# Performance work log

Hardware: AMD Instinct MI355X
Metric: run time of the kernel (lower is better)

The kernel has to match this reference:

```python
import jax, jax.numpy as jnp
import numpy as np

# Larq ste_sign: forward sign(x) with sign(0)=+1; backward is identity clipped to |x|<=1 (STE).
@jax.custom_vjp
def ste_sign(x):
    return jnp.where(x >= 0, jnp.ones((), x.dtype), -jnp.ones((), x.dtype))

def _ste_fwd(x):
    return ste_sign(x), x

def _ste_bwd(x, g):
    return (g * (jnp.abs(x) <= 1).astype(g.dtype),)

ste_sign.defvjp(_ste_fwd, _ste_bwd)


def setup_inputs() -> dict:
    key = jax.random.key(0)
    k1, k2 = jax.random.split(key)
    x = jax.random.normal(k1, (16, 112, 112, 256), dtype=jnp.float32)      # NHWC
    kernel = jax.random.normal(k2, (3, 3, 256, 1), dtype=jnp.float32) * 0.1  # (kh, kw, C, mult)
    return {"x": x, "kernel": kernel}


def reference(x, kernel):
    # Quantize input and depthwise kernel, then standard depthwise conv (stride 1, SAME, no bias).
    xq = ste_sign(x)
    kq = ste_sign(kernel)
    kh, kw, C, mult = kernel.shape
    rhs = kq.reshape(kh, kw, 1, C * mult)  # HWIO layout for grouped conv
    out = jax.lax.conv_general_dilated(
        xq, rhs,
        window_strides=(1, 1),
        padding="SAME",
        feature_group_count=C,
        dimension_numbers=("NHWC", "HWIO", "NHWC"),
    )
    return out
```

## Files before the change

### kernel.cpp

```cpp
#include <hip/hip_runtime.h>


constexpr int N = 16, H = 112, W = 112, C = 256;
constexpr int TW = 16;

typedef float f32x4 __attribute__((ext_vector_type(4)));

template<bool TOP, bool BOT>
__device__ __forceinline__ void run_strip(
        const float* __restrict__ x, const float* __restrict__ k,
        float* __restrict__ out, int n, int h, int w0, int c0) {

    constexpr unsigned VMASK = (TOP ? 0x1u : 0u) | 0x8u | (BOT ? 0x40u : 0u);
    constexpr int NROWS = (TOP ? 1 : 0) + 1 + (BOT ? 1 : 0);

    unsigned kb[4] = {0u, 0u, 0u, 0u};
#pragma unroll
    for (int t = 0; t < 9; ++t) {
        const uint4 kv = *reinterpret_cast<const uint4*>(k + t * C + c0);
        kb[0] |= (kv.x >> 31) << t;
        kb[1] |= (kv.y >> 31) << t;
        kb[2] |= (kv.z >> 31) << t;
        kb[3] |= (kv.w >> 31) << t;
    }
    unsigned kbj[3][4];
#pragma unroll
    for (int j = 0; j < 3; ++j)
#pragma unroll
        for (int ch = 0; ch < 4; ++ch)
            kbj[j][ch] = (kb[ch] >> j) & 0x49u & VMASK;

    const size_t rowstride = (size_t)W * C;
    const float* rc = x + (size_t)(n * H + h) * rowstride + c0;
    const float* rm = rc - rowstride;
    const float* rp = rc + rowstride;
    float* orow = out + (size_t)(n * H + h) * rowstride + c0;

    auto colD = [&](int cc, int dj[3][4]) {
        uint4 xm = make_uint4(0,0,0,0), xp = make_uint4(0,0,0,0);
        if constexpr (TOP) xm = *reinterpret_cast<const uint4*>(rm + (size_t)cc * C);
        const uint4 xc = *reinterpret_cast<const uint4*>(rc + (size_t)cc * C);
        if constexpr (BOT) xp = *reinterpret_cast<const uint4*>(rp + (size_t)cc * C);

        unsigned xcode[4];
        {
            const unsigned* m = &xm.x; const unsigned* c = &xc.x; const unsigned* p = &xp.x;
#pragma unroll
            for (int ch = 0; ch < 4; ++ch) {
                unsigned r = (c[ch] >> 31) << 3;
                if constexpr (TOP) r |= (m[ch] >> 31);
                if constexpr (BOT) r |= (p[ch] >> 31) << 6;
                xcode[ch] = r;
            }
        }
#pragma unroll
        for (int ch = 0; ch < 4; ++ch)
#pragma unroll
            for (int j = 0; j < 3; ++j)
                dj[j][ch] = NROWS - 2 * __popc(xcode[ch] ^ kbj[j][ch]);
    };

    int d0_m2[4], d0_m1[4], d1_m1[4];

    if (w0 > 0) {
        int dj[3][4]; colD(w0 - 1, dj);
#pragma unroll
        for (int ch = 0; ch < 4; ++ch) d0_m2[ch] = dj[0][ch];
    } else {
#pragma unroll
        for (int ch = 0; ch < 4; ++ch) d0_m2[ch] = 0;
    }
    {
        int dj[3][4]; colD(w0, dj);
#pragma unroll
        for (int ch = 0; ch < 4; ++ch) { d0_m1[ch] = dj[0][ch]; d1_m1[ch] = dj[1][ch]; }
    }

#pragma unroll 3
    for (int i = 1; i < TW; ++i) {
        const int cc = w0 + i;
        int dj[3][4]; colD(cc, dj);
        f32x4 ov;
#pragma unroll
        for (int ch = 0; ch < 4; ++ch) {
            ov[ch] = (float)(d0_m2[ch] + d1_m1[ch] + dj[2][ch]);
            d0_m2[ch] = d0_m1[ch]; d0_m1[ch] = dj[0][ch]; d1_m1[ch] = dj[1][ch];
        }
        __builtin_nontemporal_store(ov,
            reinterpret_cast<f32x4*>(orow + (size_t)(cc - 1) * C));
    }

    {
        const int cc = w0 + TW;
        int d2v[4] = {0, 0, 0, 0};
        if (cc < W) {
            int dj[3][4]; colD(cc, dj);
#pragma unroll
            for (int ch = 0; ch < 4; ++ch) d2v[ch] = dj[2][ch];
        }
        f32x4 ov;
#pragma unroll
        for (int ch = 0; ch < 4; ++ch) ov[ch] = (float)(d0_m2[ch] + d1_m1[ch] + d2v[ch]);
        __builtin_nontemporal_store(ov,
            reinterpret_cast<f32x4*>(orow + (size_t)(cc - 1) * C));
    }
}

__global__ __launch_bounds__(256) void bsign_dw3x3_pop(
        const float* __restrict__ x, const float* __restrict__ k,
        float* __restrict__ out) {
    const int c0 = (threadIdx.x & 63) << 2;
    const int wq = threadIdx.x >> 6;
    const int h  = blockIdx.y * 4 + wq;
    const int w0 = blockIdx.x * TW;
    const int n  = blockIdx.z;

    if (h == 0)            run_strip<false, true >(x, k, out, n, h, w0, c0);
    else if (h == H - 1)   run_strip<true,  false>(x, k, out, n, h, w0, c0);
    else                   run_strip<true,  true >(x, k, out, n, h, w0, c0);
}

extern "C" void kernel_launch(void* const* d_in, const int* in_sizes, int n_in,
                              void* d_out, int out_size, void* d_ws, size_t ws_size,
                              hipStream_t stream) {
    const float* x = (const float*)d_in[0];
    const float* k = (const float*)d_in[1];
    float* out = (float*)d_out;

    dim3 grid(W / TW, H / 4, N);
    bsign_dw3x3_pop<<<grid, 256, 0, stream>>>(x, k, out);
}
```

Measured before the change: 351.3 us.

## Register-block four output rows per thread to cut vertical input re-reads

New measurement: 362.2 us. 1.03x slower.

```diff
diff --git a/kernel.cpp b/kernel.cpp
--- a/kernel.cpp
+++ b/kernel.cpp
@@ -2,122 +2,117 @@
 
 
 constexpr int N = 16, H = 112, W = 112, C = 256;
-constexpr int TW = 16;
+constexpr int TW = 8;
+constexpr int R  = 4;
 
 typedef float f32x4 __attribute__((ext_vector_type(4)));
 
+struct TrueT  { static constexpr bool value = true;  };
+struct FalseT { static constexpr bool value = false; };
+
 template<bool TOP, bool BOT>
-__device__ __forceinline__ void run_strip(
+__device__ __forceinline__ void run_tile(
         const float* __restrict__ x, const float* __restrict__ k,
-        float* __restrict__ out, int n, int h, int w0, int c0) {
+        float* __restrict__ out, int n, int h0, int w0, int c0) {
 
-    constexpr unsigned VMASK = (TOP ? 0x1u : 0u) | 0x8u | (BOT ? 0x40u : 0u);
-    constexpr int NROWS = (TOP ? 1 : 0) + 1 + (BOT ? 1 : 0);
-
-    unsigned kb[4] = {0u, 0u, 0u, 0u};
+    unsigned kj3[3][4] = {{0,0,0,0},{0,0,0,0},{0,0,0,0}};
 #pragma unroll
     for (int t = 0; t < 9; ++t) {
         const uint4 kv = *reinterpret_cast<const uint4*>(k + t * C + c0);
-        kb[0] |= (kv.x >> 31) << t;
-        kb[1] |= (kv.y >> 31) << t;
-        kb[2] |= (kv.z >> 31) << t;
-        kb[3] |= (kv.w >> 31) << t;
+        const int kr = t / 3, kj = t % 3;
+        kj3[kj][0] |= (kv.x >> 31) << kr;
+        kj3[kj][1] |= (kv.y >> 31) << kr;
+        kj3[kj][2] |= (kv.z >> 31) << kr;
+        kj3[kj][3] |= (kv.w >> 31) << kr;
     }
-    unsigned kbj[3][4];
-#pragma unroll
-    for (int j = 0; j < 3; ++j)
-#pragma unroll
-        for (int ch = 0; ch < 4; ++ch)
-            kbj[j][ch] = (kb[ch] >> j) & 0x49u & VMASK;
+
+    constexpr int PLO = TOP ? 1 : 0;
+    constexpr int PHI = BOT ? R : R + 1;
 
     const size_t rowstride = (size_t)W * C;
-    const float* rc = x + (size_t)(n * H + h) * rowstride + c0;
-    const float* rm = rc - rowstride;
-    const float* rp = rc + rowstride;
-    float* orow = out + (size_t)(n * H + h) * rowstride + c0;
+    const float* xin = x + (size_t)(n * H + (h0 - 1)) * rowstride + c0;
+    float* o0 = out + (size_t)(n * H + h0) * rowstride + c0;
 
-    auto colD = [&](int cc, int dj[3][4]) {
-        uint4 xm = make_uint4(0,0,0,0), xp = make_uint4(0,0,0,0);
-        if constexpr (TOP) xm = *reinterpret_cast<const uint4*>(rm + (size_t)cc * C);
-        const uint4 xc = *reinterpret_cast<const uint4*>(rc + (size_t)cc * C);
-        if constexpr (BOT) xp = *reinterpret_cast<const uint4*>(rp + (size_t)cc * C);
+    auto colSig = [&](int cc, unsigned rs[4]) {
+        rs[0] = rs[1] = rs[2] = rs[3] = 0u;
+        const float* cp = xin + (size_t)cc * C;
+#pragma unroll
+        for (int p = PLO; p <= PHI; ++p) {
+            const uint4 v = *reinterpret_cast<const uint4*>(cp + (size_t)p * rowstride);
+            rs[0] |= (v.x >> 31) << p;
+            rs[1] |= (v.y >> 31) << p;
+            rs[2] |= (v.z >> 31) << p;
+            rs[3] |= (v.w >> 31) << p;
+        }
+    };
 
-        unsigned xcode[4];
-        {
-            const unsigned* m = &xm.x; const unsigned* c = &xc.x; const unsigned* p = &xp.x;
+    auto emit = [&](int w, const unsigned rs0[4], const unsigned rs1[4],
+                    const unsigned rs2[4], auto h0t, auto h2t) {
+#pragma unroll
+        for (int r = 0; r < R; ++r) {
+            constexpr_if_workaround:;
+            const bool border = (TOP && r == 0) || (BOT && r == R - 1);
+            const unsigned msk = (TOP && r == 0) ? 0x6u
+                               : (BOT && r == R - 1) ? 0x3u : 0x7u;
+            const int nr = border ? 2 : 3;
+            f32x4 ov;
 #pragma unroll
             for (int ch = 0; ch < 4; ++ch) {
-                unsigned r = (c[ch] >> 31) << 3;
-                if constexpr (TOP) r |= (m[ch] >> 31);
-                if constexpr (BOT) r |= (p[ch] >> 31) << 6;
-                xcode[ch] = r;
+                int cnt = 0, nt = 0;
+                if constexpr (decltype(h0t)::value) {
+                    cnt += __popc(((rs0[ch] >> r) ^ kj3[0][ch]) & msk); nt += nr;
+                }
+                cnt += __popc(((rs1[ch] >> r) ^ kj3[1][ch]) & msk); nt += nr;
+                if constexpr (decltype(h2t)::value) {
+                    cnt += __popc(((rs2[ch] >> r) ^ kj3[2][ch]) & msk); nt += nr;
+                }
+                ov[ch] = (float)(nt - 2 * cnt);
             }
+            __builtin_nontemporal_store(ov,
+                reinterpret_cast<f32x4*>(o0 + (size_t)r * rowstride + (size_t)w * C));
         }
-#pragma unroll
-        for (int ch = 0; ch < 4; ++ch)
-#pragma unroll
-            for (int j = 0; j < 3; ++j)
-                dj[j][ch] = NROWS - 2 * __popc(xcode[ch] ^ kbj[j][ch]);
     };
 
-    int d0_m2[4], d0_m1[4], d1_m1[4];
+    unsigned rs_m2[4], rs_m1[4], rs_c[4];
 
-    if (w0 > 0) {
-        int dj[3][4]; colD(w0 - 1, dj);
+    if (w0 > 0) colSig(w0 - 1, rs_m2);
+    else        { rs_m2[0] = rs_m2[1] = rs_m2[2] = rs_m2[3] = 0u; }
+    colSig(w0, rs_m1);
+
+    colSig(w0 + 1, rs_c);
+    if (w0 > 0) emit(w0, rs_m2, rs_m1, rs_c, TrueT{},  TrueT{});
+    else        emit(w0, rs_m2, rs_m1, rs_c, FalseT{}, TrueT{});
 #pragma unroll
-        for (int ch = 0; ch < 4; ++ch) d0_m2[ch] = dj[0][ch];
-    } else {
+    for (int ch = 0; ch < 4; ++ch) { rs_m2[ch] = rs_m1[ch]; rs_m1[ch] = rs_c[ch]; }
+
+#pragma unroll 3
+    for (int i = 2; i < TW; ++i) {
+        colSig(w0 + i, rs_c);
+        emit(w0 + i - 1, rs_m2, rs_m1, rs_c, TrueT{}, TrueT{});
 #pragma unroll
-        for (int ch = 0; ch < 4; ++ch) d0_m2[ch] = 0;
-    }
-    {
-        int dj[3][4]; colD(w0, dj);
-#pragma unroll
-        for (int ch = 0; ch < 4; ++ch) { d0_m1[ch] = dj[0][ch]; d1_m1[ch] = dj[1][ch]; }
+        for (int ch = 0; ch < 4; ++ch) { rs_m2[ch] = rs_m1[ch]; rs_m1[ch] = rs_c[ch]; }
     }
 
-#pragma unroll 3
-    for (int i = 1; i < TW; ++i) {
-        const int cc = w0 + i;
-        int dj[3][4]; colD(cc, dj);
-        f32x4 ov;
-#pragma unroll
-        for (int ch = 0; ch < 4; ++ch) {
-            ov[ch] = (float)(d0_m2[ch] + d1_m1[ch] + dj[2][ch]);
-            d0_m2[ch] = d0_m1[ch]; d0_m1[ch] = dj[0][ch]; d1_m1[ch] = dj[1][ch];
-        }
-        __builtin_nontemporal_store(ov,
-            reinterpret_cast<f32x4*>(orow + (size_t)(cc - 1) * C));
-    }
-
-    {
-        const int cc = w0 + TW;
-        int d2v[4] = {0, 0, 0, 0};
-        if (cc < W) {
-            int dj[3][4]; colD(cc, dj);
-#pragma unroll
-            for (int ch = 0; ch < 4; ++ch) d2v[ch] = dj[2][ch];
-        }
-        f32x4 ov;
-#pragma unroll
-        for (int ch = 0; ch < 4; ++ch) ov[ch] = (float)(d0_m2[ch] + d1_m1[ch] + d2v[ch]);
-        __builtin_nontemporal_store(ov,
-            reinterpret_cast<f32x4*>(orow + (size_t)(cc - 1) * C));
+    if (w0 + TW < W) {
+        colSig(w0 + TW, rs_c);
+        emit(w0 + TW - 1, rs_m2, rs_m1, rs_c, TrueT{}, TrueT{});
+    } else {
+        emit(w0 + TW - 1, rs_m2, rs_m1, rs_c, TrueT{}, FalseT{});
     }
 }
 
-__global__ __launch_bounds__(256) void bsign_dw3x3_pop(
+__global__ __launch_bounds__(256) void bsign_dw3x3_r4(
         const float* __restrict__ x, const float* __restrict__ k,
         float* __restrict__ out) {
     const int c0 = (threadIdx.x & 63) << 2;
     const int wq = threadIdx.x >> 6;
-    const int h  = blockIdx.y * 4 + wq;
+    const int h0 = blockIdx.y * (4 * R) + wq * R;
     const int w0 = blockIdx.x * TW;
     const int n  = blockIdx.z;
 
-    if (h == 0)            run_strip<false, true >(x, k, out, n, h, w0, c0);
-    else if (h == H - 1)   run_strip<true,  false>(x, k, out, n, h, w0, c0);
-    else                   run_strip<true,  true >(x, k, out, n, h, w0, c0);
+    if (h0 == 0)           run_tile<true,  false>(x, k, out, n, h0, w0, c0);
+    else if (h0 == H - R)  run_tile<false, true >(x, k, out, n, h0, w0, c0);
+    else                   run_tile<false, false>(x, k, out, n, h0, w0, c0);
 }
 
 extern "C" void kernel_launch(void* const* d_in, const int* in_sizes, int n_in,
@@ -127,6 +122,6 @@
     const float* k = (const float*)d_in[1];
     float* out = (float*)d_out;
 
-    dim3 grid(W / TW, H / 4, N);
-    bsign_dw3x3_pop<<<grid, 256, 0, stream>>>(x, k, out);
+    dim3 grid(W / TW, H / (4 * R), N);
+    bsign_dw3x3_r4<<<grid, 256, 0, stream>>>(x, k, out);
 }
```
